# Kernel tuning notes

Measured on AMD Instinct MI355X. Metric: run time of the kernel, lower is better.

Reference implementation:

```python
import jax, jax.numpy as jnp
import numpy as np

B, N_ATOMS, N_ALIGN = 65536, 128, 64


def setup_inputs() -> dict:
    key = jax.random.key(0)
    k1, k2 = jax.random.split(key)
    traj = jax.random.normal(k1, (B, N_ATOMS, 3), dtype=jnp.float32)
    ref_pos = jax.random.normal(k2, (N_ATOMS, 3), dtype=jnp.float32)
    align_idx = jnp.arange(N_ALIGN, dtype=jnp.int32)  # 0-based (ids - 1)
    return {"traj": traj, "ref_pos": ref_pos, "align_idx": align_idx}


def reference(traj, ref_pos, align_idx):
    # --- __init__: centered reference coordinates of alignment atoms ---
    ref_x = ref_pos[align_idx]                      # [K, 3]
    ref_x = ref_x - jnp.mean(ref_x, axis=0)         # center

    # --- forward: Kabsch alignment per frame ---
    sel = traj[:, align_idx, :]                     # [B, K, 3]
    x_c = jnp.mean(sel, axis=1, keepdims=True)      # [B, 1, 3]
    x_notran = sel - x_c                            # [B, K, 3]
    # xtmp = x_notran^T  -> prod[b] = x_notran[b]^T @ ref_x : [B, 3, 3]
    prod = jnp.einsum('bki,kj->bij', x_notran, ref_x)

    u, s, vh = jnp.linalg.svd(prod)                 # u,vh: [B, 3, 3]
    sign_vec = jnp.sign(jnp.linalg.det(u @ vh))     # [B]
    # diag(1, 1, sign) applied on the right of u
    d = jnp.stack([jnp.ones_like(sign_vec), jnp.ones_like(sign_vec), sign_vec], axis=-1)
    rotate_mat = (u * d[:, None, :]) @ vh           # [B, 3, 3]

    aligned_traj = jnp.matmul(traj - x_c, rotate_mat)  # [B, N, 3]
    return aligned_traj
```

## Files before the change

kernel.cpp:

```cpp
#include <hip/hip_runtime.h>
#include <math.h>

#define NATOMS 128
#define NALIGN 64
#define FPB    8
#define TPB    256

#define JACOBI_ROT(app, aqq, apq, arp, arq, pcol, qcol)                 \
  {                                                                     \
    float _apq = (apq);                                                 \
    if (fabsf(_apq) > 1e-20f) {                                         \
      float _tau = ((aqq) - (app)) / (2.0f * _apq);                     \
      float _t = (_tau >= 0.0f ? 1.0f : -1.0f) /                        \
                 (fabsf(_tau) + sqrtf(1.0f + _tau * _tau));             \
      float _c = rsqrtf(1.0f + _t * _t);                                \
      float _s = _t * _c;                                               \
      (app) -= _t * _apq;                                               \
      (aqq) += _t * _apq;                                               \
      (apq) = 0.0f;                                                     \
      float _rp = (arp), _rq = (arq);                                   \
      (arp) = _c * _rp - _s * _rq;                                      \
      (arq) = _s * _rp + _c * _rq;                                      \
      _Pragma("unroll")                                                 \
      for (int _r = 0; _r < 3; _r++) {                                  \
        float _vp = v[3 * _r + (pcol)], _vq = v[3 * _r + (qcol)];       \
        v[3 * _r + (pcol)] = _c * _vp - _s * _vq;                       \
        v[3 * _r + (qcol)] = _s * _vp + _c * _vq;                       \
      }                                                                 \
    }                                                                   \
  }

__global__ __launch_bounds__(TPB) void align_kernel(
    const float* __restrict__ traj,
    const float* __restrict__ ref_pos,
    const int* __restrict__ align_idx,
    float* __restrict__ out,
    int B)
{
    __shared__ float4 s_rmap[NATOMS];
    __shared__ __align__(16) float s_mat[FPB][12];

    const int t  = threadIdx.x;
    const int f0 = blockIdx.x * FPB;
    const int f  = t >> 5;
    const int r  = t & 31;
    const int gf = f0 + f;
    const bool valid = (gf < B);

    float4 q0, q1, q2;
    if (valid) {
        const float* p = traj + (size_t)gf * (NATOMS * 3) + r * 12;
        q0 = *(const float4*)(p);
        q1 = *(const float4*)(p + 4);
        q2 = *(const float4*)(p + 8);
    } else {
        q0 = q1 = q2 = make_float4(0.f, 0.f, 0.f, 0.f);
    }

    if (t < NALIGN) {
        const float4 z4 = make_float4(0.f, 0.f, 0.f, 0.f);
        s_rmap[t]          = z4;
        s_rmap[t + NALIGN] = z4;

        int idx = align_idx[t];
        float rx = ref_pos[idx * 3 + 0];
        float ry = ref_pos[idx * 3 + 1];
        float rz = ref_pos[idx * 3 + 2];
        float sx = rx, sy = ry, sz = rz;
        #pragma unroll
        for (int off = 32; off >= 1; off >>= 1) {
            sx += __shfl_xor(sx, off);
            sy += __shfl_xor(sy, off);
            sz += __shfl_xor(sz, off);
        }
        const float inv = 1.0f / (float)NALIGN;
        int slot = ((idx & 3) << 5) | (idx >> 2);
        s_rmap[slot] = make_float4(rx - sx * inv, ry - sy * inv, rz - sz * inv, 1.0f);
    }
    __syncthreads();

    float xx[4] = { q0.x, q0.w, q1.z, q2.y };
    float yy[4] = { q0.y, q1.x, q1.w, q2.z };
    float zz[4] = { q0.z, q1.y, q2.x, q2.w };

    {
        float sx = 0.f, sy = 0.f, sz = 0.f;
        float c[9] = {0.f,0.f,0.f,0.f,0.f,0.f,0.f,0.f,0.f};
        #pragma unroll
        for (int j = 0; j < 4; j++) {
            float4 rm = s_rmap[(j << 5) | r];
            sx += rm.w * xx[j]; sy += rm.w * yy[j]; sz += rm.w * zz[j];
            c[0] += xx[j]*rm.x; c[1] += xx[j]*rm.y; c[2] += xx[j]*rm.z;
            c[3] += yy[j]*rm.x; c[4] += yy[j]*rm.y; c[5] += yy[j]*rm.z;
            c[6] += zz[j]*rm.x; c[7] += zz[j]*rm.y; c[8] += zz[j]*rm.z;
        }
        #pragma unroll
        for (int off = 16; off >= 1; off >>= 1) {
            sx += __shfl_xor(sx, off);
            sy += __shfl_xor(sy, off);
            sz += __shfl_xor(sz, off);
            #pragma unroll
            for (int jj = 0; jj < 9; jj++) c[jj] += __shfl_xor(c[jj], off);
        }
        if (r == 0 && valid) {
            #pragma unroll
            for (int jj = 0; jj < 9; jj++) s_mat[f][jj] = c[jj];
            const float inv = 1.0f / (float)NALIGN;
            s_mat[f][9]  = sx * inv;
            s_mat[f][10] = sy * inv;
            s_mat[f][11] = sz * inv;
        }
    }
    __syncthreads();

    if (t < FPB && (f0 + t) < B) {
        float m[9];
        #pragma unroll
        for (int j = 0; j < 9; j++) m[j] = s_mat[t][j];

        float a00 = m[0]*m[0] + m[3]*m[3] + m[6]*m[6];
        float a01 = m[0]*m[1] + m[3]*m[4] + m[6]*m[7];
        float a02 = m[0]*m[2] + m[3]*m[5] + m[6]*m[8];
        float a11 = m[1]*m[1] + m[4]*m[4] + m[7]*m[7];
        float a12 = m[1]*m[2] + m[4]*m[5] + m[7]*m[8];
        float a22 = m[2]*m[2] + m[5]*m[5] + m[8]*m[8];

        float v[9] = {1.f,0.f,0.f, 0.f,1.f,0.f, 0.f,0.f,1.f};
        #pragma unroll
        for (int sweep = 0; sweep < 5; sweep++) {
            JACOBI_ROT(a00, a11, a01, a02, a12, 0, 1);
            JACOBI_ROT(a00, a22, a02, a01, a12, 0, 2);
            JACOBI_ROT(a11, a22, a12, a01, a02, 1, 2);
        }

        float dd[3] = {a00, a11, a22};
        #pragma unroll
        for (int pass = 0; pass < 3; pass++) {
            int ii = (pass == 0) ? 0 : (pass == 1) ? 0 : 1;
            int jj = (pass == 0) ? 1 : 2;
            if (dd[ii] < dd[jj]) {
                float tmp = dd[ii]; dd[ii] = dd[jj]; dd[jj] = tmp;
                #pragma unroll
                for (int rr = 0; rr < 3; rr++) {
                    float tv = v[3*rr+ii]; v[3*rr+ii] = v[3*rr+jj]; v[3*rr+jj] = tv;
                }
            }
        }

        float v0x = v[0], v0y = v[3], v0z = v[6];
        float v1x = v[1], v1y = v[4], v1z = v[7];
        float v2x = v[2], v2y = v[5], v2z = v[8];

        float u1x = m[0]*v0x + m[1]*v0y + m[2]*v0z;
        float u1y = m[3]*v0x + m[4]*v0y + m[5]*v0z;
        float u1z = m[6]*v0x + m[7]*v0y + m[8]*v0z;
        float n1 = rsqrtf(fmaxf(u1x*u1x + u1y*u1y + u1z*u1z, 1e-30f));
        u1x *= n1; u1y *= n1; u1z *= n1;

        float u2x = m[0]*v1x + m[1]*v1y + m[2]*v1z;
        float u2y = m[3]*v1x + m[4]*v1y + m[5]*v1z;
        float u2z = m[6]*v1x + m[7]*v1y + m[8]*v1z;
        float d12 = u1x*u2x + u1y*u2y + u1z*u2z;
        u2x -= d12 * u1x; u2y -= d12 * u1y; u2z -= d12 * u1z;
        float n2 = rsqrtf(fmaxf(u2x*u2x + u2y*u2y + u2z*u2z, 1e-30f));
        u2x *= n2; u2y *= n2; u2z *= n2;

        float u3x = u1y*u2z - u1z*u2y;
        float u3y = u1z*u2x - u1x*u2z;
        float u3z = u1x*u2y - u1y*u2x;
        float cx = v1y*v2z - v1z*v2y;
        float cy = v1z*v2x - v1x*v2z;
        float cz = v1x*v2y - v1y*v2x;
        float detv = v0x*cx + v0y*cy + v0z*cz;
        float sg = (detv >= 0.f) ? 1.f : -1.f;
        u3x *= sg; u3y *= sg; u3z *= sg;

        s_mat[t][0] = u1x*v0x + u2x*v1x + u3x*v2x;
        s_mat[t][1] = u1x*v0y + u2x*v1y + u3x*v2y;
        s_mat[t][2] = u1x*v0z + u2x*v1z + u3x*v2z;
        s_mat[t][3] = u1y*v0x + u2y*v1x + u3y*v2x;
        s_mat[t][4] = u1y*v0y + u2y*v1y + u3y*v2y;
        s_mat[t][5] = u1y*v0z + u2y*v1z + u3y*v2z;
        s_mat[t][6] = u1z*v0x + u2z*v1x + u3z*v2x;
        s_mat[t][7] = u1z*v0y + u2z*v1y + u3z*v2y;
        s_mat[t][8] = u1z*v0z + u2z*v1z + u3z*v2z;
    }
    __syncthreads();

    if (valid) {
        float4 Ra = *(const float4*)&s_mat[f][0];
        float4 Rb = *(const float4*)&s_mat[f][4];
        float4 Rc = *(const float4*)&s_mat[f][8];
        float R0 = Ra.x, R1 = Ra.y, R2 = Ra.z, R3 = Ra.w;
        float R4 = Rb.x, R5 = Rb.y, R6 = Rb.z, R7 = Rb.w;
        float R8 = Rc.x, xcx = Rc.y, xcy = Rc.z, xcz = Rc.w;

        float ox[4], oy[4], oz[4];
        #pragma unroll
        for (int j = 0; j < 4; j++) {
            float dx = xx[j] - xcx, dy = yy[j] - xcy, dz = zz[j] - xcz;
            ox[j] = dx*R0 + dy*R3 + dz*R6;
            oy[j] = dx*R1 + dy*R4 + dz*R7;
            oz[j] = dx*R2 + dy*R5 + dz*R8;
        }

        float* po = out + (size_t)gf * (NATOMS * 3) + r * 12;
        *(float4*)(po)     = make_float4(ox[0], oy[0], oz[0], ox[1]);
        *(float4*)(po + 4) = make_float4(oy[1], oz[1], ox[2], oy[2]);
        *(float4*)(po + 8) = make_float4(oz[2], ox[3], oy[3], oz[3]);
    }
}

extern "C" void kernel_launch(void* const* d_in, const int* in_sizes, int n_in,
                              void* d_out, int out_size, void* d_ws, size_t ws_size,
                              hipStream_t stream) {
    const float* traj      = (const float*)d_in[0];
    const float* ref_pos   = (const float*)d_in[1];
    const int*   align_idx = (const int*)d_in[2];
    float*       out       = (float*)d_out;

    int B = in_sizes[0] / (NATOMS * 3);
    int grid = (B + FPB - 1) / FPB;
    align_kernel<<<grid, TPB, 0, stream>>>(traj, ref_pos, align_idx, out, B);
}
```

Before: 190.4 us.

## Split alignment into covariance/SVD kernel and apply kernel via workspace

When workspace is available, the fused kernel is split in two. The first kernel computes per-frame covariance and centroid with 8 threads per frame, then runs the Jacobi SVD for 64 frames per block in parallel threads and writes a rotation matrix to the workspace. The second kernel re-reads the trajectory and applies the rotation. The aim is to parallelize the serial SVD stage that stalled the fused blocks. The cost is that the alignment atoms are read twice, with an extra kernel launch and a workspace round-trip. The fused fallback now runs the SVD on lane 0 of each warp instead of in a separate phase.

```diff
diff --git a/kernel.cpp b/kernel.cpp
--- a/kernel.cpp
+++ b/kernel.cpp
@@ -3,8 +3,11 @@
 
 #define NATOMS 128
 #define NALIGN 64
-#define FPB    8
-#define TPB    256
+
+#define TPB1   512
+#define FPW    64
+#define TPB2   256
+#define FPB2   8
 
 #define JACOBI_ROT(app, aqq, apq, arp, arq, pcol, qcol)                 \
   {                                                                     \
@@ -30,7 +33,216 @@
     }                                                                   \
   }
 
-__global__ __launch_bounds__(TPB) void align_kernel(
+__device__ __forceinline__ void svd_rotation(const float* m, float xcx, float xcy,
+                                             float xcz, float* dst)
+{
+    float a00 = m[0]*m[0] + m[3]*m[3] + m[6]*m[6];
+    float a01 = m[0]*m[1] + m[3]*m[4] + m[6]*m[7];
+    float a02 = m[0]*m[2] + m[3]*m[5] + m[6]*m[8];
+    float a11 = m[1]*m[1] + m[4]*m[4] + m[7]*m[7];
+    float a12 = m[1]*m[2] + m[4]*m[5] + m[7]*m[8];
+    float a22 = m[2]*m[2] + m[5]*m[5] + m[8]*m[8];
+
+    float v[9] = {1.f,0.f,0.f, 0.f,1.f,0.f, 0.f,0.f,1.f};
+    #pragma unroll
+    for (int sweep = 0; sweep < 5; sweep++) {
+        JACOBI_ROT(a00, a11, a01, a02, a12, 0, 1);
+        JACOBI_ROT(a00, a22, a02, a01, a12, 0, 2);
+        JACOBI_ROT(a11, a22, a12, a01, a02, 1, 2);
+    }
+
+    float dd[3] = {a00, a11, a22};
+    #pragma unroll
+    for (int pass = 0; pass < 3; pass++) {
+        int ii = (pass == 0) ? 0 : (pass == 1) ? 0 : 1;
+        int jj = (pass == 0) ? 1 : 2;
+        if (dd[ii] < dd[jj]) {
+            float tmp = dd[ii]; dd[ii] = dd[jj]; dd[jj] = tmp;
+            #pragma unroll
+            for (int rr = 0; rr < 3; rr++) {
+                float tv = v[3*rr+ii]; v[3*rr+ii] = v[3*rr+jj]; v[3*rr+jj] = tv;
+            }
+        }
+    }
+
+    float v0x = v[0], v0y = v[3], v0z = v[6];
+    float v1x = v[1], v1y = v[4], v1z = v[7];
+    float v2x = v[2], v2y = v[5], v2z = v[8];
+
+    float u1x = m[0]*v0x + m[1]*v0y + m[2]*v0z;
+    float u1y = m[3]*v0x + m[4]*v0y + m[5]*v0z;
+    float u1z = m[6]*v0x + m[7]*v0y + m[8]*v0z;
+    float n1 = rsqrtf(fmaxf(u1x*u1x + u1y*u1y + u1z*u1z, 1e-30f));
+    u1x *= n1; u1y *= n1; u1z *= n1;
+
+    float u2x = m[0]*v1x + m[1]*v1y + m[2]*v1z;
+    float u2y = m[3]*v1x + m[4]*v1y + m[5]*v1z;
+    float u2z = m[6]*v1x + m[7]*v1y + m[8]*v1z;
+    float d12 = u1x*u2x + u1y*u2y + u1z*u2z;
+    u2x -= d12 * u1x; u2y -= d12 * u1y; u2z -= d12 * u1z;
+    float n2 = rsqrtf(fmaxf(u2x*u2x + u2y*u2y + u2z*u2z, 1e-30f));
+    u2x *= n2; u2y *= n2; u2z *= n2;
+
+    float u3x = u1y*u2z - u1z*u2y;
+    float u3y = u1z*u2x - u1x*u2z;
+    float u3z = u1x*u2y - u1y*u2x;
+    float cx = v1y*v2z - v1z*v2y;
+    float cy = v1z*v2x - v1x*v2z;
+    float cz = v1x*v2y - v1y*v2x;
+    float detv = v0x*cx + v0y*cy + v0z*cz;
+    float sg = (detv >= 0.f) ? 1.f : -1.f;
+    u3x *= sg; u3y *= sg; u3z *= sg;
+
+    dst[0] = u1x*v0x + u2x*v1x + u3x*v2x;
+    dst[1] = u1x*v0y + u2x*v1y + u3x*v2y;
+    dst[2] = u1x*v0z + u2x*v1z + u3x*v2z;
+    dst[3] = u1y*v0x + u2y*v1x + u3y*v2x;
+    dst[4] = u1y*v0y + u2y*v1y + u3y*v2y;
+    dst[5] = u1y*v0z + u2y*v1z + u3y*v2z;
+    dst[6] = u1z*v0x + u2z*v1x + u3z*v2x;
+    dst[7] = u1z*v0y + u2z*v1y + u3z*v2y;
+    dst[8] = u1z*v0z + u2z*v1z + u3z*v2z;
+    dst[9]  = xcx;
+    dst[10] = xcy;
+    dst[11] = xcz;
+}
+
+__global__ __launch_bounds__(TPB1) void cov_svd_kernel(
+    const float* __restrict__ traj,
+    const float* __restrict__ ref_pos,
+    const int* __restrict__ align_idx,
+    float* __restrict__ rmat,
+    int B)
+{
+    __shared__ float4 s_ref[NALIGN];
+    __shared__ int    s_idx[NALIGN];
+    __shared__ float  s_cov[FPW][13];
+
+    const int t = threadIdx.x;
+
+    if (t < NALIGN) {
+        int idx = align_idx[t];
+        s_idx[t] = idx;
+        float rx = ref_pos[idx * 3 + 0];
+        float ry = ref_pos[idx * 3 + 1];
+        float rz = ref_pos[idx * 3 + 2];
+        float sx = rx, sy = ry, sz = rz;
+        #pragma unroll
+        for (int off = 32; off >= 1; off >>= 1) {
+            sx += __shfl_xor(sx, off);
+            sy += __shfl_xor(sy, off);
+            sz += __shfl_xor(sz, off);
+        }
+        const float inv = 1.0f / (float)NALIGN;
+        s_ref[t] = make_float4(rx - sx * inv, ry - sy * inv, rz - sz * inv, 0.0f);
+    }
+    __syncthreads();
+
+    {
+        const int f   = t >> 3;
+        const int sub = t & 7;
+        const int gf  = blockIdx.x * FPW + f;
+        if (gf < B) {
+            const float* fr = traj + (size_t)gf * (NATOMS * 3);
+            float sx = 0.f, sy = 0.f, sz = 0.f;
+            float c[9] = {0.f,0.f,0.f,0.f,0.f,0.f,0.f,0.f,0.f};
+            #pragma unroll
+            for (int i = 0; i < 8; i++) {
+                int a   = sub + 8 * i;
+                int idx = s_idx[a];
+                float x = fr[idx * 3 + 0];
+                float y = fr[idx * 3 + 1];
+                float z = fr[idx * 3 + 2];
+                float4 r = s_ref[a];
+                sx += x; sy += y; sz += z;
+                c[0] += x * r.x; c[1] += x * r.y; c[2] += x * r.z;
+                c[3] += y * r.x; c[4] += y * r.y; c[5] += y * r.z;
+                c[6] += z * r.x; c[7] += z * r.y; c[8] += z * r.z;
+            }
+            #pragma unroll
+            for (int off = 4; off >= 1; off >>= 1) {
+                sx += __shfl_xor(sx, off);
+                sy += __shfl_xor(sy, off);
+                sz += __shfl_xor(sz, off);
+                #pragma unroll
+                for (int j = 0; j < 9; j++) c[j] += __shfl_xor(c[j], off);
+            }
+            if (sub == 0) {
+                #pragma unroll
+                for (int j = 0; j < 9; j++) s_cov[f][j] = c[j];
+                const float inv = 1.0f / (float)NALIGN;
+                s_cov[f][9]  = sx * inv;
+                s_cov[f][10] = sy * inv;
+                s_cov[f][11] = sz * inv;
+            }
+        }
+    }
+    __syncthreads();
+
+    if (t < FPW) {
+        int gf = blockIdx.x * FPW + t;
+        if (gf < B) {
+            float m[9];
+            #pragma unroll
+            for (int j = 0; j < 9; j++) m[j] = s_cov[t][j];
+            float res[12];
+            svd_rotation(m, s_cov[t][9], s_cov[t][10], s_cov[t][11], res);
+            float4* dst = (float4*)(rmat + (size_t)gf * 12);
+            dst[0] = make_float4(res[0], res[1], res[2],  res[3]);
+            dst[1] = make_float4(res[4], res[5], res[6],  res[7]);
+            dst[2] = make_float4(res[8], res[9], res[10], res[11]);
+        }
+    }
+}
+
+__global__ __launch_bounds__(TPB2) void apply_kernel(
+    const float* __restrict__ traj,
+    const float* __restrict__ rmat,
+    float* __restrict__ out,
+    int B)
+{
+    const int t  = threadIdx.x;
+    const int f  = t >> 5;
+    const int r  = t & 31;
+    const int gf = blockIdx.x * FPB2 + f;
+    if (gf >= B) return;
+
+    const float* p = traj + (size_t)gf * (NATOMS * 3) + r * 12;
+    float4 q0 = *(const float4*)(p);
+    float4 q1 = *(const float4*)(p + 4);
+    float4 q2 = *(const float4*)(p + 8);
+
+    const float4* Rt = (const float4*)(rmat + (size_t)gf * 12);
+    float4 Ra = Rt[0], Rb = Rt[1], Rc = Rt[2];
+    float R0 = Ra.x, R1 = Ra.y, R2 = Ra.z, R3 = Ra.w;
+    float R4 = Rb.x, R5 = Rb.y, R6 = Rb.z, R7 = Rb.w;
+    float R8 = Rc.x, xcx = Rc.y, xcy = Rc.z, xcz = Rc.w;
+
+    float dx, dy, dz;
+    dx = q0.x - xcx; dy = q0.y - xcy; dz = q0.z - xcz;
+    float o0x = dx*R0 + dy*R3 + dz*R6;
+    float o0y = dx*R1 + dy*R4 + dz*R7;
+    float o0z = dx*R2 + dy*R5 + dz*R8;
+    dx = q0.w - xcx; dy = q1.x - xcy; dz = q1.y - xcz;
+    float o1x = dx*R0 + dy*R3 + dz*R6;
+    float o1y = dx*R1 + dy*R4 + dz*R7;
+    float o1z = dx*R2 + dy*R5 + dz*R8;
+    dx = q1.z - xcx; dy = q1.w - xcy; dz = q2.x - xcz;
+    float o2x = dx*R0 + dy*R3 + dz*R6;
+    float o2y = dx*R1 + dy*R4 + dz*R7;
+    float o2z = dx*R2 + dy*R5 + dz*R8;
+    dx = q2.y - xcx; dy = q2.z - xcy; dz = q2.w - xcz;
+    float o3x = dx*R0 + dy*R3 + dz*R6;
+    float o3y = dx*R1 + dy*R4 + dz*R7;
+    float o3z = dx*R2 + dy*R5 + dz*R8;
+
+    float* po = out + (size_t)gf * (NATOMS * 3) + r * 12;
+    *(float4*)(po)     = make_float4(o0x, o0y, o0z, o1x);
+    *(float4*)(po + 4) = make_float4(o1y, o1z, o2x, o2y);
+    *(float4*)(po + 8) = make_float4(o2z, o3x, o3y, o3z);
+}
+
+__global__ __launch_bounds__(256) void align_fused_kernel(
     const float* __restrict__ traj,
     const float* __restrict__ ref_pos,
     const int* __restrict__ align_idx,
@@ -38,10 +250,10 @@
     int B)
 {
     __shared__ float4 s_rmap[NATOMS];
-    __shared__ __align__(16) float s_mat[FPB][12];
+    __shared__ __align__(16) float s_mat[8][12];
 
     const int t  = threadIdx.x;
-    const int f0 = blockIdx.x * FPB;
+    const int f0 = blockIdx.x * 8;
     const int f  = t >> 5;
     const int r  = t & 31;
     const int gf = f0 + f;
@@ -61,7 +273,6 @@
         const float4 z4 = make_float4(0.f, 0.f, 0.f, 0.f);
         s_rmap[t]          = z4;
         s_rmap[t + NALIGN] = z4;
-
         int idx = align_idx[t];
         float rx = ref_pos[idx * 3 + 0];
         float ry = ref_pos[idx * 3 + 1];
@@ -103,87 +314,12 @@
             for (int jj = 0; jj < 9; jj++) c[jj] += __shfl_xor(c[jj], off);
         }
         if (r == 0 && valid) {
-            #pragma unroll
-            for (int jj = 0; jj < 9; jj++) s_mat[f][jj] = c[jj];
+            float res[12];
             const float inv = 1.0f / (float)NALIGN;
-            s_mat[f][9]  = sx * inv;
-            s_mat[f][10] = sy * inv;
-            s_mat[f][11] = sz * inv;
-        }
-    }
-    __syncthreads();
-
-    if (t < FPB && (f0 + t) < B) {
-        float m[9];
-        #pragma unroll
-        for (int j = 0; j < 9; j++) m[j] = s_mat[t][j];
-
-        float a00 = m[0]*m[0] + m[3]*m[3] + m[6]*m[6];
-        float a01 = m[0]*m[1] + m[3]*m[4] + m[6]*m[7];
-        float a02 = m[0]*m[2] + m[3]*m[5] + m[6]*m[8];
-        float a11 = m[1]*m[1] + m[4]*m[4] + m[7]*m[7];
-        float a12 = m[1]*m[2] + m[4]*m[5] + m[7]*m[8];
-        float a22 = m[2]*m[2] + m[5]*m[5] + m[8]*m[8];
-
-        float v[9] = {1.f,0.f,0.f, 0.f,1.f,0.f, 0.f,0.f,1.f};
-        #pragma unroll
-        for (int sweep = 0; sweep < 5; sweep++) {
-            JACOBI_ROT(a00, a11, a01, a02, a12, 0, 1);
-            JACOBI_ROT(a00, a22, a02, a01, a12, 0, 2);
-            JACOBI_ROT(a11, a22, a12, a01, a02, 1, 2);
-        }
-
-        float dd[3] = {a00, a11, a22};
-        #pragma unroll
-        for (int pass = 0; pass < 3; pass++) {
-            int ii = (pass == 0) ? 0 : (pass == 1) ? 0 : 1;
-            int jj = (pass == 0) ? 1 : 2;
-            if (dd[ii] < dd[jj]) {
-                float tmp = dd[ii]; dd[ii] = dd[jj]; dd[jj] = tmp;
-                #pragma unroll
-                for (int rr = 0; rr < 3; rr++) {
-                    float tv = v[3*rr+ii]; v[3*rr+ii] = v[3*rr+jj]; v[3*rr+jj] = tv;
-                }
-            }
-        }
-
-        float v0x = v[0], v0y = v[3], v0z = v[6];
-        float v1x = v[1], v1y = v[4], v1z = v[7];
-        float v2x = v[2], v2y = v[5], v2z = v[8];
-
-        float u1x = m[0]*v0x + m[1]*v0y + m[2]*v0z;
-        float u1y = m[3]*v0x + m[4]*v0y + m[5]*v0z;
-        float u1z = m[6]*v0x + m[7]*v0y + m[8]*v0z;
-        float n1 = rsqrtf(fmaxf(u1x*u1x + u1y*u1y + u1z*u1z, 1e-30f));
-        u1x *= n1; u1y *= n1; u1z *= n1;
-
-        float u2x = m[0]*v1x + m[1]*v1y + m[2]*v1z;
-        float u2y = m[3]*v1x + m[4]*v1y + m[5]*v1z;
-        float u2z = m[6]*v1x + m[7]*v1y + m[8]*v1z;
-        float d12 = u1x*u2x + u1y*u2y + u1z*u2z;
-        u2x -= d12 * u1x; u2y -= d12 * u1y; u2z -= d12 * u1z;
-        float n2 = rsqrtf(fmaxf(u2x*u2x + u2y*u2y + u2z*u2z, 1e-30f));
-        u2x *= n2; u2y *= n2; u2z *= n2;
-
-        float u3x = u1y*u2z - u1z*u2y;
-        float u3y = u1z*u2x - u1x*u2z;
-        float u3z = u1x*u2y - u1y*u2x;
-        float cx = v1y*v2z - v1z*v2y;
-        float cy = v1z*v2x - v1x*v2z;
-        float cz = v1x*v2y - v1y*v2x;
-        float detv = v0x*cx + v0y*cy + v0z*cz;
-        float sg = (detv >= 0.f) ? 1.f : -1.f;
-        u3x *= sg; u3y *= sg; u3z *= sg;
-
-        s_mat[t][0] = u1x*v0x + u2x*v1x + u3x*v2x;
-        s_mat[t][1] = u1x*v0y + u2x*v1y + u3x*v2y;
-        s_mat[t][2] = u1x*v0z + u2x*v1z + u3x*v2z;
-        s_mat[t][3] = u1y*v0x + u2y*v1x + u3y*v2x;
-        s_mat[t][4] = u1y*v0y + u2y*v1y + u3y*v2y;
-        s_mat[t][5] = u1y*v0z + u2y*v1z + u3y*v2z;
-        s_mat[t][6] = u1z*v0x + u2z*v1x + u3z*v2x;
-        s_mat[t][7] = u1z*v0y + u2z*v1y + u3z*v2y;
-        s_mat[t][8] = u1z*v0z + u2z*v1z + u3z*v2z;
+            svd_rotation(c, sx * inv, sy * inv, sz * inv, res);
+            #pragma unroll
+            for (int jj = 0; jj < 12; jj++) s_mat[f][jj] = res[jj];
+        }
     }
     __syncthreads();
 
@@ -203,7 +339,6 @@
             oy[j] = dx*R1 + dy*R4 + dz*R7;
             oz[j] = dx*R2 + dy*R5 + dz*R8;
         }
-
         float* po = out + (size_t)gf * (NATOMS * 3) + r * 12;
         *(float4*)(po)     = make_float4(ox[0], oy[0], oz[0], ox[1]);
         *(float4*)(po + 4) = make_float4(oy[1], oz[1], ox[2], oy[2]);
@@ -220,6 +355,16 @@
     float*       out       = (float*)d_out;
 
     int B = in_sizes[0] / (NATOMS * 3);
-    int grid = (B + FPB - 1) / FPB;
-    align_kernel<<<grid, TPB, 0, stream>>>(traj, ref_pos, align_idx, out, B);
-}
+    size_t need = (size_t)B * 12 * sizeof(float);
+
+    if (d_ws != nullptr && ws_size >= need) {
+        float* rmat = (float*)d_ws;
+        int grid1 = (B + FPW - 1) / FPW;
+        cov_svd_kernel<<<grid1, TPB1, 0, stream>>>(traj, ref_pos, align_idx, rmat, B);
+        int grid2 = (B + FPB2 - 1) / FPB2;
+        apply_kernel<<<grid2, TPB2, 0, stream>>>(traj, rmat, out, B);
+    } else {
+        int grid = (B + 7) / 8;
+        align_fused_kernel<<<grid, 256, 0, stream>>>(traj, ref_pos, align_idx, out, B);
+    }
+}
```

New measurement: 198.2 us. 1.04x slower.

## Compute SVD redundantly in every lane to drop shared-memory handoff and barriers

Applied to the files above, without the earlier changes.

After the butterfly reduction every lane already holds the full 3x3 covariance and centroid. Each lane now runs the Jacobi eigen-solve and builds the rotation itself, instead of one thread per frame doing it and passing results through shared memory with two __syncthreads. The Jacobi rotation and the sort are made branchless (clamped denominator, selects) so lanes stay uniform. This removes the serial single-lane section and the barriers, at the cost of doing the solve 32 times redundantly per frame and using more registers.

```diff
diff --git a/kernel.cpp b/kernel.cpp
--- a/kernel.cpp
+++ b/kernel.cpp
@@ -9,24 +9,24 @@
 #define JACOBI_ROT(app, aqq, apq, arp, arq, pcol, qcol)                 \
   {                                                                     \
     float _apq = (apq);                                                 \
-    if (fabsf(_apq) > 1e-20f) {                                         \
-      float _tau = ((aqq) - (app)) / (2.0f * _apq);                     \
-      float _t = (_tau >= 0.0f ? 1.0f : -1.0f) /                        \
-                 (fabsf(_tau) + sqrtf(1.0f + _tau * _tau));             \
-      float _c = rsqrtf(1.0f + _t * _t);                                \
-      float _s = _t * _c;                                               \
-      (app) -= _t * _apq;                                               \
-      (aqq) += _t * _apq;                                               \
-      (apq) = 0.0f;                                                     \
-      float _rp = (arp), _rq = (arq);                                   \
-      (arp) = _c * _rp - _s * _rq;                                      \
-      (arq) = _s * _rp + _c * _rq;                                      \
-      _Pragma("unroll")                                                 \
-      for (int _r = 0; _r < 3; _r++) {                                  \
-        float _vp = v[3 * _r + (pcol)], _vq = v[3 * _r + (qcol)];       \
-        v[3 * _r + (pcol)] = _c * _vp - _s * _vq;                       \
-        v[3 * _r + (qcol)] = _s * _vp + _c * _vq;                       \
-      }                                                                 \
+    float _den = 2.0f * _apq;                                           \
+    _den = copysignf(fmaxf(fabsf(_den), 1e-30f), _den);                 \
+    float _tau = ((aqq) - (app)) / _den;                                \
+    float _t = (_tau >= 0.0f ? 1.0f : -1.0f) /                          \
+               (fabsf(_tau) + sqrtf(1.0f + _tau * _tau));               \
+    float _c = rsqrtf(1.0f + _t * _t);                                  \
+    float _s = _t * _c;                                                 \
+    (app) -= _t * _apq;                                                 \
+    (aqq) += _t * _apq;                                                 \
+    (apq) = 0.0f;                                                      \
+    float _rp = (arp), _rq = (arq);                                     \
+    (arp) = _c * _rp - _s * _rq;                                        \
+    (arq) = _s * _rp + _c * _rq;                                        \
+    _Pragma("unroll")                                                   \
+    for (int _r = 0; _r < 3; _r++) {                                    \
+      float _vp = v[3 * _r + (pcol)], _vq = v[3 * _r + (qcol)];         \
+      v[3 * _r + (pcol)] = _c * _vp - _s * _vq;                         \
+      v[3 * _r + (qcol)] = _s * _vp + _c * _vq;                         \
     }                                                                   \
   }
 
@@ -38,7 +38,6 @@
     int B)
 {
     __shared__ float4 s_rmap[NATOMS];
-    __shared__ __align__(16) float s_mat[FPB][12];
 
     const int t  = threadIdx.x;
     const int f0 = blockIdx.x * FPB;
@@ -83,118 +82,100 @@
     float yy[4] = { q0.y, q1.x, q1.w, q2.z };
     float zz[4] = { q0.z, q1.y, q2.x, q2.w };
 
-    {
-        float sx = 0.f, sy = 0.f, sz = 0.f;
-        float c[9] = {0.f,0.f,0.f,0.f,0.f,0.f,0.f,0.f,0.f};
-        #pragma unroll
-        for (int j = 0; j < 4; j++) {
-            float4 rm = s_rmap[(j << 5) | r];
-            sx += rm.w * xx[j]; sy += rm.w * yy[j]; sz += rm.w * zz[j];
-            c[0] += xx[j]*rm.x; c[1] += xx[j]*rm.y; c[2] += xx[j]*rm.z;
-            c[3] += yy[j]*rm.x; c[4] += yy[j]*rm.y; c[5] += yy[j]*rm.z;
-            c[6] += zz[j]*rm.x; c[7] += zz[j]*rm.y; c[8] += zz[j]*rm.z;
+    float sx = 0.f, sy = 0.f, sz = 0.f;
+    float c[9] = {0.f,0.f,0.f,0.f,0.f,0.f,0.f,0.f,0.f};
+    #pragma unroll
+    for (int j = 0; j < 4; j++) {
+        float4 rm = s_rmap[(j << 5) | r];
+        sx += rm.w * xx[j]; sy += rm.w * yy[j]; sz += rm.w * zz[j];
+        c[0] += xx[j]*rm.x; c[1] += xx[j]*rm.y; c[2] += xx[j]*rm.z;
+        c[3] += yy[j]*rm.x; c[4] += yy[j]*rm.y; c[5] += yy[j]*rm.z;
+        c[6] += zz[j]*rm.x; c[7] += zz[j]*rm.y; c[8] += zz[j]*rm.z;
+    }
+    #pragma unroll
+    for (int off = 16; off >= 1; off >>= 1) {
+        sx += __shfl_xor(sx, off);
+        sy += __shfl_xor(sy, off);
+        sz += __shfl_xor(sz, off);
+        #pragma unroll
+        for (int jj = 0; jj < 9; jj++) c[jj] += __shfl_xor(c[jj], off);
+    }
+    const float invA = 1.0f / (float)NALIGN;
+    const float xcx = sx * invA, xcy = sy * invA, xcz = sz * invA;
+
+    const float* m = c;
+
+    float a00 = m[0]*m[0] + m[3]*m[3] + m[6]*m[6];
+    float a01 = m[0]*m[1] + m[3]*m[4] + m[6]*m[7];
+    float a02 = m[0]*m[2] + m[3]*m[5] + m[6]*m[8];
+    float a11 = m[1]*m[1] + m[4]*m[4] + m[7]*m[7];
+    float a12 = m[1]*m[2] + m[4]*m[5] + m[7]*m[8];
+    float a22 = m[2]*m[2] + m[5]*m[5] + m[8]*m[8];
+
+    float v[9] = {1.f,0.f,0.f, 0.f,1.f,0.f, 0.f,0.f,1.f};
+    #pragma unroll
+    for (int sweep = 0; sweep < 5; sweep++) {
+        JACOBI_ROT(a00, a11, a01, a02, a12, 0, 1);
+        JACOBI_ROT(a00, a22, a02, a01, a12, 0, 2);
+        JACOBI_ROT(a11, a22, a12, a01, a02, 1, 2);
+    }
+
+    float dd[3] = {a00, a11, a22};
+    #pragma unroll
+    for (int pass = 0; pass < 3; pass++) {
+        const int ii = (pass == 2) ? 1 : 0;
+        const int jj = (pass == 0) ? 1 : 2;
+        float di = dd[ii], dj = dd[jj];
+        bool sw = di < dj;
+        dd[ii] = sw ? dj : di;
+        dd[jj] = sw ? di : dj;
+        #pragma unroll
+        for (int rr = 0; rr < 3; rr++) {
+            float a = v[3*rr+ii], b = v[3*rr+jj];
+            v[3*rr+ii] = sw ? b : a;
+            v[3*rr+jj] = sw ? a : b;
         }
-        #pragma unroll
-        for (int off = 16; off >= 1; off >>= 1) {
-            sx += __shfl_xor(sx, off);
-            sy += __shfl_xor(sy, off);
-            sz += __shfl_xor(sz, off);
-            #pragma unroll
-            for (int jj = 0; jj < 9; jj++) c[jj] += __shfl_xor(c[jj], off);
-        }
-        if (r == 0 && valid) {
-            #pragma unroll
-            for (int jj = 0; jj < 9; jj++) s_mat[f][jj] = c[jj];
-            const float inv = 1.0f / (float)NALIGN;
-            s_mat[f][9]  = sx * inv;
-            s_mat[f][10] = sy * inv;
-            s_mat[f][11] = sz * inv;
-        }
-    }
-    __syncthreads();
-
-    if (t < FPB && (f0 + t) < B) {
-        float m[9];
-        #pragma unroll
-        for (int j = 0; j < 9; j++) m[j] = s_mat[t][j];
-
-        float a00 = m[0]*m[0] + m[3]*m[3] + m[6]*m[6];
-        float a01 = m[0]*m[1] + m[3]*m[4] + m[6]*m[7];
-        float a02 = m[0]*m[2] + m[3]*m[5] + m[6]*m[8];
-        float a11 = m[1]*m[1] + m[4]*m[4] + m[7]*m[7];
-        float a12 = m[1]*m[2] + m[4]*m[5] + m[7]*m[8];
-        float a22 = m[2]*m[2] + m[5]*m[5] + m[8]*m[8];
-
-        float v[9] = {1.f,0.f,0.f, 0.f,1.f,0.f, 0.f,0.f,1.f};
-        #pragma unroll
-        for (int sweep = 0; sweep < 5; sweep++) {
-            JACOBI_ROT(a00, a11, a01, a02, a12, 0, 1);
-            JACOBI_ROT(a00, a22, a02, a01, a12, 0, 2);
-            JACOBI_ROT(a11, a22, a12, a01, a02, 1, 2);
-        }
-
-        float dd[3] = {a00, a11, a22};
-        #pragma unroll
-        for (int pass = 0; pass < 3; pass++) {
-            int ii = (pass == 0) ? 0 : (pass == 1) ? 0 : 1;
-            int jj = (pass == 0) ? 1 : 2;
-            if (dd[ii] < dd[jj]) {
-                float tmp = dd[ii]; dd[ii] = dd[jj]; dd[jj] = tmp;
-                #pragma unroll
-                for (int rr = 0; rr < 3; rr++) {
-                    float tv = v[3*rr+ii]; v[3*rr+ii] = v[3*rr+jj]; v[3*rr+jj] = tv;
-                }
-            }
-        }
-
-        float v0x = v[0], v0y = v[3], v0z = v[6];
-        float v1x = v[1], v1y = v[4], v1z = v[7];
-        float v2x = v[2], v2y = v[5], v2z = v[8];
-
-        float u1x = m[0]*v0x + m[1]*v0y + m[2]*v0z;
-        float u1y = m[3]*v0x + m[4]*v0y + m[5]*v0z;
-        float u1z = m[6]*v0x + m[7]*v0y + m[8]*v0z;
-        float n1 = rsqrtf(fmaxf(u1x*u1x + u1y*u1y + u1z*u1z, 1e-30f));
-        u1x *= n1; u1y *= n1; u1z *= n1;
-
-        float u2x = m[0]*v1x + m[1]*v1y + m[2]*v1z;
-        float u2y = m[3]*v1x + m[4]*v1y + m[5]*v1z;
-        float u2z = m[6]*v1x + m[7]*v1y + m[8]*v1z;
-        float d12 = u1x*u2x + u1y*u2y + u1z*u2z;
-        u2x -= d12 * u1x; u2y -= d12 * u1y; u2z -= d12 * u1z;
-        float n2 = rsqrtf(fmaxf(u2x*u2x + u2y*u2y + u2z*u2z, 1e-30f));
-        u2x *= n2; u2y *= n2; u2z *= n2;
-
-        float u3x = u1y*u2z - u1z*u2y;
-        float u3y = u1z*u2x - u1x*u2z;
-        float u3z = u1x*u2y - u1y*u2x;
-        float cx = v1y*v2z - v1z*v2y;
-        float cy = v1z*v2x - v1x*v2z;
-        float cz = v1x*v2y - v1y*v2x;
-        float detv = v0x*cx + v0y*cy + v0z*cz;
-        float sg = (detv >= 0.f) ? 1.f : -1.f;
-        u3x *= sg; u3y *= sg; u3z *= sg;
-
-        s_mat[t][0] = u1x*v0x + u2x*v1x + u3x*v2x;
-        s_mat[t][1] = u1x*v0y + u2x*v1y + u3x*v2y;
-        s_mat[t][2] = u1x*v0z + u2x*v1z + u3x*v2z;
-        s_mat[t][3] = u1y*v0x + u2y*v1x + u3y*v2x;
-        s_mat[t][4] = u1y*v0y + u2y*v1y + u3y*v2y;
-        s_mat[t][5] = u1y*v0z + u2y*v1z + u3y*v2z;
-        s_mat[t][6] = u1z*v0x + u2z*v1x + u3z*v2x;
-        s_mat[t][7] = u1z*v0y + u2z*v1y + u3z*v2y;
-        s_mat[t][8] = u1z*v0z + u2z*v1z + u3z*v2z;
-    }
-    __syncthreads();
+    }
+
+    float v0x = v[0], v0y = v[3], v0z = v[6];
+    float v1x = v[1], v1y = v[4], v1z = v[7];
+    float v2x = v[2], v2y = v[5], v2z = v[8];
+
+    float u1x = m[0]*v0x + m[1]*v0y + m[2]*v0z;
+    float u1y = m[3]*v0x + m[4]*v0y + m[5]*v0z;
+    float u1z = m[6]*v0x + m[7]*v0y + m[8]*v0z;
+    float n1 = rsqrtf(fmaxf(u1x*u1x + u1y*u1y + u1z*u1z, 1e-30f));
+    u1x *= n1; u1y *= n1; u1z *= n1;
+
+    float u2x = m[0]*v1x + m[1]*v1y + m[2]*v1z;
+    float u2y = m[3]*v1x + m[4]*v1y + m[5]*v1z;
+    float u2z = m[6]*v1x + m[7]*v1y + m[8]*v1z;
+    float d12 = u1x*u2x + u1y*u2y + u1z*u2z;
+    u2x -= d12 * u1x; u2y -= d12 * u1y; u2z -= d12 * u1z;
+    float n2 = rsqrtf(fmaxf(u2x*u2x + u2y*u2y + u2z*u2z, 1e-30f));
+    u2x *= n2; u2y *= n2; u2z *= n2;
+
+    float u3x = u1y*u2z - u1z*u2y;
+    float u3y = u1z*u2x - u1x*u2z;
+    float u3z = u1x*u2y - u1y*u2x;
+    float cxv = v1y*v2z - v1z*v2y;
+    float cyv = v1z*v2x - v1x*v2z;
+    float czv = v1x*v2y - v1y*v2x;
+    float detv = v0x*cxv + v0y*cyv + v0z*czv;
+    float sg = (detv >= 0.f) ? 1.f : -1.f;
+    u3x *= sg; u3y *= sg; u3z *= sg;
+
+    float R0 = u1x*v0x + u2x*v1x + u3x*v2x;
+    float R1 = u1x*v0y + u2x*v1y + u3x*v2y;
+    float R2 = u1x*v0z + u2x*v1z + u3x*v2z;
+    float R3 = u1y*v0x + u2y*v1x + u3y*v2x;
+    float R4 = u1y*v0y + u2y*v1y + u3y*v2y;
+    float R5 = u1y*v0z + u2y*v1z + u3y*v2z;
+    float R6 = u1z*v0x + u2z*v1x + u3z*v2x;
+    float R7 = u1z*v0y + u2z*v1y + u3z*v2y;
+    float R8 = u1z*v0z + u2z*v1z + u3z*v2z;
 
     if (valid) {
-        float4 Ra = *(const float4*)&s_mat[f][0];
-        float4 Rb = *(const float4*)&s_mat[f][4];
-        float4 Rc = *(const float4*)&s_mat[f][8];
-        float R0 = Ra.x, R1 = Ra.y, R2 = Ra.z, R3 = Ra.w;
-        float R4 = Rb.x, R5 = Rb.y, R6 = Rb.z, R7 = Rb.w;
-        float R8 = Rc.x, xcx = Rc.y, xcy = Rc.z, xcz = Rc.w;
-
         float ox[4], oy[4], oz[4];
         #pragma unroll
         for (int j = 0; j < 4; j++) {
```

Result: slower. 215.2 us (+13.0%).
